# Kernel tuning notes

Measured on AMD Instinct MI355X. Metric: run time of the kernel, lower is better.

The kernel has to match this reference:

```python
import jax, jax.numpy as jnp
import numpy as np

TOK_DIM = 512
POS_DIM = 512
N_HEADS = 16
HEAD_DIM = 64
D_MODEL = 1024
INNER = N_HEADS * HEAD_DIM
B, T = 4, 2048


def setup_inputs() -> dict:
    key = jax.random.key(0)
    ks = jax.random.split(key, 5)
    s = 0.02
    return {
        "x": jax.random.normal(ks[0], (B, T, TOK_DIM + POS_DIM), dtype=jnp.float32),
        "Wq": jax.random.normal(ks[1], (POS_DIM, INNER), dtype=jnp.float32) * s,
        "Wk": jax.random.normal(ks[2], (POS_DIM, INNER), dtype=jnp.float32) * s,
        "Wv": jax.random.normal(ks[3], (TOK_DIM, INNER), dtype=jnp.float32) * s,
        "Wo": jax.random.normal(ks[4], (INNER, D_MODEL), dtype=jnp.float32) * s,
    }


def reference(x, Wq, Wk, Wv, Wo):
    b, t, _ = x.shape
    x_tok = x[:, :, :TOK_DIM]
    x_pos = x[:, :, TOK_DIM:]
    # project and split heads: [B, H, T, Dh]
    q = (x_pos @ Wq).reshape(b, t, N_HEADS, HEAD_DIM).transpose(0, 2, 1, 3)
    k = (x_pos @ Wk).reshape(b, t, N_HEADS, HEAD_DIM).transpose(0, 2, 1, 3)
    v = (x_tok @ Wv).reshape(b, t, N_HEADS, HEAD_DIM).transpose(0, 2, 1, 3)
    att = jnp.einsum("bhqd,bhkd->bhqk", q, k) / jnp.sqrt(jnp.float32(HEAD_DIM))
    causal = jnp.tril(jnp.ones((t, t), dtype=bool))
    att = jnp.where(causal, att, -jnp.inf)
    att = jax.nn.softmax(att, axis=-1)
    out = jnp.einsum("bhqk,bhkd->bhqd", att, v)
    out = out.transpose(0, 2, 1, 3).reshape(b, t, INNER)
    return out @ Wo
```

## Files before the change

### kernel.cpp

```cpp
#include <hip/hip_runtime.h>
#include <stdint.h>


typedef unsigned short u16;
typedef __bf16 bf16;
typedef bf16 bf16x8 __attribute__((ext_vector_type(8)));
typedef u16 u16x8 __attribute__((ext_vector_type(8)));
typedef u16 u16x4 __attribute__((ext_vector_type(4)));
typedef float f32x4 __attribute__((ext_vector_type(4)));
typedef uint32_t u32x4 __attribute__((ext_vector_type(4)));

__device__ __forceinline__ u16 cvt_bf16(float f) {
  uint32_t u = __builtin_bit_cast(uint32_t, f);
  u += 0x7FFFu + ((u >> 16) & 1u);
  return (u16)(u >> 16);
}

__device__ __forceinline__ uint32_t pack2_bf16(float lo, float hi) {
  uint32_t a = __builtin_bit_cast(uint32_t, lo) + 0x8000u;
  uint32_t b = __builtin_bit_cast(uint32_t, hi) + 0x8000u;
  return __builtin_amdgcn_perm(b, a, 0x07060302u);
}

__device__ __forceinline__ f32x4 mfma_bf(bf16x8 a, bf16x8 b, f32x4 c) {
  return __builtin_amdgcn_mfma_f32_16x16x32_bf16(a, b, c, 0, 0, 0);
}

typedef __attribute__((address_space(1))) const uint32_t g_u32;
typedef __attribute__((address_space(3))) uint32_t l_u32;
__device__ __forceinline__ void gload16(const u16* g, u16* l) {
  __builtin_amdgcn_global_load_lds((g_u32*)g, (l_u32*)l, 16, 0, 0);
}

__global__ __launch_bounds__(256) void prep_x(
    const float* __restrict__ x, u16* __restrict__ xtok,
    u16* __restrict__ xpos) {
  int idx = blockIdx.x * 256 + threadIdx.x;
  int row = idx >> 8;
  int c4 = (idx & 255) * 4;
  float4 v = *(const float4*)(x + (size_t)row * 1024 + c4);
  u16x4 b = {cvt_bf16(v.x), cvt_bf16(v.y), cvt_bf16(v.z), cvt_bf16(v.w)};
  u16* dst = (c4 < 512) ? (xtok + (size_t)row * 512 + c4)
                        : (xpos + (size_t)row * 512 + c4 - 512);
  *(u16x4*)dst = b;
}

__global__ __launch_bounds__(256) void prep_w(
    const float* __restrict__ Wq, const float* __restrict__ Wk,
    const float* __restrict__ Wv, const float* __restrict__ Wo,
    u16* __restrict__ Wt, u16* __restrict__ WoT) {
  const int z = blockIdx.z;
  const float* src = (z == 0) ? Wq : (z == 1) ? Wk : (z == 2) ? Wv : Wo;
  const int K = (z == 3) ? 1024 : 512;
  u16* dst = (z == 3) ? WoT : (Wt + (size_t)z * 1024 * 512);
  const int k0 = blockIdx.y * 64, n0 = blockIdx.x * 64;
  if (k0 >= K) return;
  __shared__ u16 T[64][68];
  const int tid = threadIdx.x;
  const int r = tid >> 4, c = (tid & 15) * 4;
#pragma unroll
  for (int i = 0; i < 4; i++) {
    float4 v = *(const float4*)(src + (size_t)(k0 + r + i * 16) * 1024 + n0 + c);
    u16x4 b = {cvt_bf16(v.x), cvt_bf16(v.y), cvt_bf16(v.z), cvt_bf16(v.w)};
    *(u16x4*)&T[r + i * 16][c] = b;
  }
  __syncthreads();
#pragma unroll
  for (int i = 0; i < 4; i++) {
    int n = r + i * 16;
    u16x4 v;
#pragma unroll
    for (int j = 0; j < 4; j++) v[j] = T[c + j][n];
    *(u16x4*)(dst + (size_t)(n0 + n) * K + k0 + c) = v;
  }
}

__global__ __launch_bounds__(256) void gemm_qkv(
    const u16* __restrict__ xtok, const u16* __restrict__ xpos,
    const u16* __restrict__ Wt, u16* __restrict__ qkv,
    u16* __restrict__ vperm) {
  const int z = blockIdx.z;
  const u16* A = (z == 2) ? xtok : xpos;
  const u16* Bt = Wt + (size_t)z * 1024 * 512;
  u16* outp = qkv + (size_t)z * (64u * 2048u * 64u);
  const float osc = (z == 0) ? 0.18033688011112042f : 1.0f;

  const int m0 = blockIdx.y * 128;
  const int n0 = blockIdx.x * 128;
  const int tid = threadIdx.x;
  const int lane = tid & 63;
  const int w = tid >> 6;
  const int wm = (w & 1) * 64;
  const int wn = (w >> 1) * 64;
  const int mrow = lane & 15;
  const int quad = lane >> 4;

  __shared__ __align__(16) u16 Ash[128 * 32];
  __shared__ __align__(16) u16 Bsh[128 * 32];

  f32x4 acc[4][4];
#pragma unroll
  for (int i = 0; i < 4; i++)
#pragma unroll
    for (int j = 0; j < 4; j++) acc[i][j] = (f32x4){0.f, 0.f, 0.f, 0.f};

  const int sr = w * 16 + (lane >> 2);
  const int sc = (lane & 3) * 8;
  const u16* gA = A + (size_t)(m0 + sr) * 512 + sc;
  const u16* gB = Bt + (size_t)(n0 + sr) * 512 + sc;
  u16* lA = Ash + sr * 32 + sc;
  u16* lB = Bsh + sr * 32 + sc;

  for (int kb = 0; kb < 512; kb += 32) {
    __syncthreads();
    gload16(gA + kb, lA);
    gload16(gA + 64 * 512 + kb, lA + 64 * 32);
    gload16(gB + kb, lB);
    gload16(gB + 64 * 512 + kb, lB + 64 * 32);
    __syncthreads();

    bf16x8 af[4], bfr[4];
#pragma unroll
    for (int mi = 0; mi < 4; mi++)
      af[mi] = *(const bf16x8*)(Ash + (wm + mi * 16 + mrow) * 32 + quad * 8);
#pragma unroll
    for (int ni = 0; ni < 4; ni++)
      bfr[ni] = *(const bf16x8*)(Bsh + (wn + ni * 16 + mrow) * 32 + quad * 8);
#pragma unroll
    for (int mi = 0; mi < 4; mi++)
#pragma unroll
      for (int ni = 0; ni < 4; ni++)
        acc[mi][ni] = mfma_bf(af[mi], bfr[ni], acc[mi][ni]);
  }

  if (z != 2) {
#pragma unroll
    for (int mi = 0; mi < 4; mi++)
#pragma unroll
      for (int ni = 0; ni < 4; ni++)
#pragma unroll
        for (int r = 0; r < 4; r++) {
          int m = m0 + wm + mi * 16 + quad * 4 + r;
          int n = n0 + wn + ni * 16 + mrow;
          int bb = m >> 11, t = m & 2047;
          int h = n >> 6, d = n & 63;
          outp[(((size_t)(bb * 16 + h)) * 2048 + t) * 64 + d] =
              cvt_bf16(acc[mi][ni][r] * osc);
        }
  } else {
#pragma unroll
    for (int mi = 0; mi < 4; mi++)
#pragma unroll
      for (int ni = 0; ni < 4; ni++)
#pragma unroll
        for (int r = 0; r < 4; r++) {
          int m = m0 + wm + mi * 16 + quad * 4 + r;
          int n = n0 + wn + ni * 16 + mrow;
          int bb = m >> 11, t = m & 2047;
          int h = n >> 6, d = n & 63;
          int k6 = t & 63;
          int pos = (k6 & 32) + ((k6 >> 4) & 1) * 4 + ((k6 >> 2) & 3) * 8 +
                    (k6 & 3);
          vperm[(((size_t)(bb * 16 + h)) * 64 + d) * 2048 + (t & ~63) + pos] =
              cvt_bf16(acc[mi][ni][r]);
        }
  }
}

__global__ __launch_bounds__(256, 4) void attn(
    const u16* __restrict__ qkv, const u16* __restrict__ vperm,
    u16* __restrict__ aout) {
  const int bh = blockIdx.x;
  const int sp = blockIdx.y;
  const int bb = bh >> 4, h = bh & 15;
  const u16* Qp = qkv + (size_t)bh * (2048 * 64);
  const u16* Kp = qkv + (size_t)(64 + bh) * (2048 * 64);
  const u16* Vp = vperm + (size_t)bh * (64 * 2048);

  __shared__ __align__(16) u16 Ksh0[64 * 32], Ksh1[64 * 32];
  __shared__ __align__(16) u16 Vsh0[64 * 32], Vsh1[64 * 32];
  __shared__ __align__(16) u16 Osh[4][16][72];

  const int tid = threadIdx.x;
  const int lane = tid & 63;
  const int w = tid >> 6;
  const int mrow = lane & 15;
  const int quad = lane >> 4;
  const int srow = w * 16 + (lane >> 2);
  const int sc = (lane & 3) * 8;

  const u16x8 onesu = {0x3F80, 0x3F80, 0x3F80, 0x3F80,
                       0x3F80, 0x3F80, 0x3F80, 0x3F80};
  const bf16x8 ones = __builtin_bit_cast(bf16x8, onesu);

  const u16* kgb = Kp + (size_t)srow * 64 + sc;
  const u16* vgb = Vp + (size_t)srow * 2048 + sc;

  for (int half = 0; half < 2; ++half) {
    const int qt = (half == 0) ? sp : 31 - sp;
    const int q0 = qt * 64;
    const int nk = qt + 1;

    const u16* qrow = Qp + (size_t)(q0 + w * 16 + mrow) * 64 + quad * 8;
    const bf16x8 qf0 = *(const bf16x8*)qrow;
    const bf16x8 qf1 = *(const bf16x8*)(qrow + 32);
    f32x4 o[4], ol;
#pragma unroll
    for (int dt = 0; dt < 4; ++dt) o[dt] = (f32x4){0.f, 0.f, 0.f, 0.f};
    ol = (f32x4){0.f, 0.f, 0.f, 0.f};

    u16x8 ka0 = *(const u16x8*)kgb;
    u16x8 ka1 = *(const u16x8*)(kgb + 32);
    u16x8 va0 = *(const u16x8*)vgb;
    u16x8 va1 = *(const u16x8*)(vgb + 32);

    for (int it = 0; it < nk; ++it) {
      __syncthreads();
      *(u16x8*)(Ksh0 + srow * 32 + sc) = ka0;
      *(u16x8*)(Ksh1 + srow * 32 + sc) = ka1;
      *(u16x8*)(Vsh0 + srow * 32 + sc) = va0;
      *(u16x8*)(Vsh1 + srow * 32 + sc) = va1;
      __syncthreads();

      if (it + 1 < nk) {
        const int kn = (it + 1) * 64;
        ka0 = *(const u16x8*)(kgb + (size_t)kn * 64);
        ka1 = *(const u16x8*)(kgb + (size_t)kn * 64 + 32);
        va0 = *(const u16x8*)(vgb + kn);
        va1 = *(const u16x8*)(vgb + kn + 32);
      }

      const int k0 = it * 64;
      f32x4 s[4];
#pragma unroll
      for (int nt = 0; nt < 4; ++nt) {
        bf16x8 kf0 = *(const bf16x8*)(Ksh0 + (nt * 16 + mrow) * 32 + quad * 8);
        bf16x8 kf1 = *(const bf16x8*)(Ksh1 + (nt * 16 + mrow) * 32 + quad * 8);
        f32x4 zz = (f32x4){0.f, 0.f, 0.f, 0.f};
        zz = mfma_bf(kf0, qf0, zz);
        zz = mfma_bf(kf1, qf1, zz);
        s[nt] = zz;
      }

      if (it == nk - 1) {
        const int q = q0 + w * 16 + mrow;
#pragma unroll
        for (int nt = 0; nt < 4; ++nt)
#pragma unroll
          for (int r = 0; r < 4; ++r)
            if (k0 + nt * 16 + quad * 4 + r > q) s[nt][r] = -1e30f;
      }
#pragma unroll
      for (int nt = 0; nt < 4; ++nt)
#pragma unroll
        for (int r = 0; r < 4; ++r)
          s[nt][r] = __builtin_amdgcn_exp2f(s[nt][r]);

      u32x4 w0 = {pack2_bf16(s[0][0], s[0][1]), pack2_bf16(s[0][2], s[0][3]),
                  pack2_bf16(s[1][0], s[1][1]), pack2_bf16(s[1][2], s[1][3])};
      u32x4 w1 = {pack2_bf16(s[2][0], s[2][1]), pack2_bf16(s[2][2], s[2][3]),
                  pack2_bf16(s[3][0], s[3][1]), pack2_bf16(s[3][2], s[3][3])};
      bf16x8 pf0 = __builtin_bit_cast(bf16x8, w0);
      bf16x8 pf1 = __builtin_bit_cast(bf16x8, w1);

      ol = mfma_bf(ones, pf0, ol);
      ol = mfma_bf(ones, pf1, ol);
#pragma unroll
      for (int dt = 0; dt < 4; ++dt) {
        bf16x8 vf0 = *(const bf16x8*)(Vsh0 + (dt * 16 + mrow) * 32 + quad * 8);
        bf16x8 vf1 = *(const bf16x8*)(Vsh1 + (dt * 16 + mrow) * 32 + quad * 8);
        o[dt] = mfma_bf(vf0, pf0, o[dt]);
        o[dt] = mfma_bf(vf1, pf1, o[dt]);
      }
    }

    const float inv = 1.f / ol[0];
#pragma unroll
    for (int dt = 0; dt < 4; ++dt)
#pragma unroll
      for (int r = 0; r < 4; ++r)
        Osh[w][mrow][dt * 16 + quad * 4 + r] = cvt_bf16(o[dt][r] * inv);
#pragma unroll
    for (int p = 0; p < 2; ++p) {
      int ql = (lane >> 3) + 8 * p;
      int ch = lane & 7;
      u16x8 v = *(const u16x8*)&Osh[w][ql][ch * 8];
      int t = q0 + w * 16 + ql;
      *(u16x8*)(aout + ((size_t)(bb * 2048 + t)) * 1024 + h * 64 + ch * 8) = v;
    }
  }
}

__global__ __launch_bounds__(256) void gemm_out(
    const u16* __restrict__ Am, const u16* __restrict__ WoT,
    float* __restrict__ out) {
  const int m0 = blockIdx.y * 128;
  const int n0 = blockIdx.x * 128;
  const int tid = threadIdx.x;
  const int lane = tid & 63;
  const int w = tid >> 6;
  const int wm = (w & 1) * 64;
  const int wn = (w >> 1) * 64;
  const int mrow = lane & 15;
  const int quad = lane >> 4;

  __shared__ __align__(16) u16 Ash[128 * 32];
  __shared__ __align__(16) u16 Bsh[128 * 32];

  f32x4 acc[4][4];
#pragma unroll
  for (int i = 0; i < 4; i++)
#pragma unroll
    for (int j = 0; j < 4; j++) acc[i][j] = (f32x4){0.f, 0.f, 0.f, 0.f};

  const int sr = w * 16 + (lane >> 2);
  const int sc = (lane & 3) * 8;
  const u16* gA = Am + (size_t)(m0 + sr) * 1024 + sc;
  const u16* gB = WoT + (size_t)(n0 + sr) * 1024 + sc;
  u16* lA = Ash + sr * 32 + sc;
  u16* lB = Bsh + sr * 32 + sc;

  for (int kb = 0; kb < 1024; kb += 32) {
    __syncthreads();
    gload16(gA + kb, lA);
    gload16(gA + 64 * 1024 + kb, lA + 64 * 32);
    gload16(gB + kb, lB);
    gload16(gB + 64 * 1024 + kb, lB + 64 * 32);
    __syncthreads();

    bf16x8 af[4], bfr[4];
#pragma unroll
    for (int mi = 0; mi < 4; mi++)
      af[mi] = *(const bf16x8*)(Ash + (wm + mi * 16 + mrow) * 32 + quad * 8);
#pragma unroll
    for (int ni = 0; ni < 4; ni++)
      bfr[ni] = *(const bf16x8*)(Bsh + (wn + ni * 16 + mrow) * 32 + quad * 8);
#pragma unroll
    for (int mi = 0; mi < 4; mi++)
#pragma unroll
      for (int ni = 0; ni < 4; ni++)
        acc[mi][ni] = mfma_bf(af[mi], bfr[ni], acc[mi][ni]);
  }

#pragma unroll
  for (int mi = 0; mi < 4; mi++)
#pragma unroll
    for (int ni = 0; ni < 4; ni++)
#pragma unroll
      for (int r = 0; r < 4; r++) {
        int m = m0 + wm + mi * 16 + quad * 4 + r;
        int n = n0 + wn + ni * 16 + mrow;
        out[(size_t)m * 1024 + n] = acc[mi][ni][r];
      }
}

extern "C" void kernel_launch(void* const* d_in, const int* in_sizes, int n_in,
                              void* d_out, int out_size, void* d_ws, size_t ws_size,
                              hipStream_t stream) {
  const float* x  = (const float*)d_in[0];
  const float* Wq = (const float*)d_in[1];
  const float* Wk = (const float*)d_in[2];
  const float* Wv = (const float*)d_in[3];
  const float* Wo = (const float*)d_in[4];

  u16* qkv   = (u16*)d_ws;
  u16* vperm = qkv + (size_t)3 * 64 * 2048 * 64;
  u16* aout  = vperm + (size_t)64 * 64 * 2048;
  u16* xtok  = aout + (size_t)8192 * 1024;
  u16* xpos  = xtok + (size_t)8192 * 512;
  u16* Wt    = xpos + (size_t)8192 * 512;
  u16* WoT   = Wt + (size_t)3 * 1024 * 512;
  float* out = (float*)d_out;

  prep_x<<<dim3(8192), dim3(256), 0, stream>>>(x, xtok, xpos);
  prep_w<<<dim3(16, 16, 4), dim3(256), 0, stream>>>(Wq, Wk, Wv, Wo, Wt, WoT);
  gemm_qkv<<<dim3(8, 64, 3), dim3(256), 0, stream>>>(xtok, xpos, Wt, qkv, vperm);
  attn<<<dim3(64, 16), dim3(256), 0, stream>>>(qkv, vperm, aout);
  gemm_out<<<dim3(8, 64), dim3(256), 0, stream>>>(aout, WoT, out);
}
```

Measured before the change: 223.6 us.

## Split attention into one block per query tile with padded LDS and vectorized V stores

The attention kernel drops the paired-tile scheme (sp and 31-sp in one block) and launches one block per query tile, giving 2048 blocks with launch bounds raised to 8 per SIMD and a single shared buffer reused for the output staging. The LDS rows for K and V are padded from 32 to 36 elements, and the load mapping is changed so lanes cover 16 rows by 4 chunks, to cut bank conflicts. The gemm_qkv V-permuted epilogue now writes four consecutive bf16 values as one 8-byte store instead of four scalar stores. The trade-off is worse load balance, since block work now grows from 1 to 32 KV tiles, and the launch bound of 8 may force register spills.

```diff
diff --git a/kernel.cpp b/kernel.cpp
--- a/kernel.cpp
+++ b/kernel.cpp
@@ -151,143 +151,145 @@
 #pragma unroll
     for (int mi = 0; mi < 4; mi++)
 #pragma unroll
-      for (int ni = 0; ni < 4; ni++)
-#pragma unroll
-        for (int r = 0; r < 4; r++) {
-          int m = m0 + wm + mi * 16 + quad * 4 + r;
-          int n = n0 + wn + ni * 16 + mrow;
-          int bb = m >> 11, t = m & 2047;
-          int h = n >> 6, d = n & 63;
-          int k6 = t & 63;
-          int pos = (k6 & 32) + ((k6 >> 4) & 1) * 4 + ((k6 >> 2) & 3) * 8 +
-                    (k6 & 3);
-          vperm[(((size_t)(bb * 16 + h)) * 64 + d) * 2048 + (t & ~63) + pos] =
-              cvt_bf16(acc[mi][ni][r]);
-        }
-  }
-}
-
-__global__ __launch_bounds__(256, 4) void attn(
+      for (int ni = 0; ni < 4; ni++) {
+        int m = m0 + wm + mi * 16 + quad * 4;
+        int n = n0 + wn + ni * 16 + mrow;
+        int bb = m >> 11, t = m & 2047;
+        int h = n >> 6, d = n & 63;
+        int k6 = t & 63;
+        int pos = (k6 & 32) + ((k6 >> 4) & 1) * 4 + ((k6 >> 2) & 3) * 8;
+        u16x4 v = {cvt_bf16(acc[mi][ni][0]), cvt_bf16(acc[mi][ni][1]),
+                   cvt_bf16(acc[mi][ni][2]), cvt_bf16(acc[mi][ni][3])};
+        *(u16x4*)(vperm + (((size_t)(bb * 16 + h)) * 64 + d) * 2048 +
+                  (t & ~63) + pos) = v;
+      }
+  }
+}
+
+__global__ __launch_bounds__(256, 8) void attn(
     const u16* __restrict__ qkv, const u16* __restrict__ vperm,
     u16* __restrict__ aout) {
   const int bh = blockIdx.x;
-  const int sp = blockIdx.y;
+  const int qt = blockIdx.y;
   const int bb = bh >> 4, h = bh & 15;
   const u16* Qp = qkv + (size_t)bh * (2048 * 64);
   const u16* Kp = qkv + (size_t)(64 + bh) * (2048 * 64);
   const u16* Vp = vperm + (size_t)bh * (64 * 2048);
 
-  __shared__ __align__(16) u16 Ksh0[64 * 32], Ksh1[64 * 32];
-  __shared__ __align__(16) u16 Vsh0[64 * 32], Vsh1[64 * 32];
-  __shared__ __align__(16) u16 Osh[4][16][72];
+  __shared__ __align__(16) u16 S[9216];
+  u16* Ksh0 = S;
+  u16* Ksh1 = S + 2304;
+  u16* Vsh0 = S + 4608;
+  u16* Vsh1 = S + 6912;
+  u16* Osh  = S;
 
   const int tid = threadIdx.x;
   const int lane = tid & 63;
   const int w = tid >> 6;
   const int mrow = lane & 15;
   const int quad = lane >> 4;
-  const int srow = w * 16 + (lane >> 2);
-  const int sc = (lane & 3) * 8;
+  const int srow = w * 16 + (lane & 15);
+  const int sch = (lane >> 4) * 8;
 
   const u16x8 onesu = {0x3F80, 0x3F80, 0x3F80, 0x3F80,
                        0x3F80, 0x3F80, 0x3F80, 0x3F80};
   const bf16x8 ones = __builtin_bit_cast(bf16x8, onesu);
 
-  const u16* kgb = Kp + (size_t)srow * 64 + sc;
-  const u16* vgb = Vp + (size_t)srow * 2048 + sc;
-
-  for (int half = 0; half < 2; ++half) {
-    const int qt = (half == 0) ? sp : 31 - sp;
-    const int q0 = qt * 64;
-    const int nk = qt + 1;
-
-    const u16* qrow = Qp + (size_t)(q0 + w * 16 + mrow) * 64 + quad * 8;
-    const bf16x8 qf0 = *(const bf16x8*)qrow;
-    const bf16x8 qf1 = *(const bf16x8*)(qrow + 32);
-    f32x4 o[4], ol;
-#pragma unroll
-    for (int dt = 0; dt < 4; ++dt) o[dt] = (f32x4){0.f, 0.f, 0.f, 0.f};
-    ol = (f32x4){0.f, 0.f, 0.f, 0.f};
-
-    u16x8 ka0 = *(const u16x8*)kgb;
-    u16x8 ka1 = *(const u16x8*)(kgb + 32);
-    u16x8 va0 = *(const u16x8*)vgb;
-    u16x8 va1 = *(const u16x8*)(vgb + 32);
-
-    for (int it = 0; it < nk; ++it) {
-      __syncthreads();
-      *(u16x8*)(Ksh0 + srow * 32 + sc) = ka0;
-      *(u16x8*)(Ksh1 + srow * 32 + sc) = ka1;
-      *(u16x8*)(Vsh0 + srow * 32 + sc) = va0;
-      *(u16x8*)(Vsh1 + srow * 32 + sc) = va1;
-      __syncthreads();
-
-      if (it + 1 < nk) {
-        const int kn = (it + 1) * 64;
-        ka0 = *(const u16x8*)(kgb + (size_t)kn * 64);
-        ka1 = *(const u16x8*)(kgb + (size_t)kn * 64 + 32);
-        va0 = *(const u16x8*)(vgb + kn);
-        va1 = *(const u16x8*)(vgb + kn + 32);
-      }
-
-      const int k0 = it * 64;
-      f32x4 s[4];
-#pragma unroll
-      for (int nt = 0; nt < 4; ++nt) {
-        bf16x8 kf0 = *(const bf16x8*)(Ksh0 + (nt * 16 + mrow) * 32 + quad * 8);
-        bf16x8 kf1 = *(const bf16x8*)(Ksh1 + (nt * 16 + mrow) * 32 + quad * 8);
-        f32x4 zz = (f32x4){0.f, 0.f, 0.f, 0.f};
-        zz = mfma_bf(kf0, qf0, zz);
-        zz = mfma_bf(kf1, qf1, zz);
-        s[nt] = zz;
-      }
-
-      if (it == nk - 1) {
-        const int q = q0 + w * 16 + mrow;
-#pragma unroll
-        for (int nt = 0; nt < 4; ++nt)
-#pragma unroll
-          for (int r = 0; r < 4; ++r)
-            if (k0 + nt * 16 + quad * 4 + r > q) s[nt][r] = -1e30f;
-      }
+  const u16* kgb = Kp + (size_t)srow * 64 + sch;
+  const u16* vgb = Vp + (size_t)srow * 2048 + sch;
+  const int lidx = srow * 36 + sch;
+
+  const int q0 = qt * 64;
+  const int nk = qt + 1;
+
+  const u16* qrow = Qp + (size_t)(q0 + w * 16 + mrow) * 64 + quad * 8;
+  const bf16x8 qf0 = *(const bf16x8*)qrow;
+  const bf16x8 qf1 = *(const bf16x8*)(qrow + 32);
+  f32x4 o[4], ol;
+#pragma unroll
+  for (int dt = 0; dt < 4; ++dt) o[dt] = (f32x4){0.f, 0.f, 0.f, 0.f};
+  ol = (f32x4){0.f, 0.f, 0.f, 0.f};
+
+  u16x8 ka0 = *(const u16x8*)kgb;
+  u16x8 ka1 = *(const u16x8*)(kgb + 32);
+  u16x8 va0 = *(const u16x8*)vgb;
+  u16x8 va1 = *(const u16x8*)(vgb + 32);
+
+  for (int it = 0; it < nk; ++it) {
+    __syncthreads();
+    *(u16x8*)(Ksh0 + lidx) = ka0;
+    *(u16x8*)(Ksh1 + lidx) = ka1;
+    *(u16x8*)(Vsh0 + lidx) = va0;
+    *(u16x8*)(Vsh1 + lidx) = va1;
+    __syncthreads();
+
+    if (it + 1 < nk) {
+      const int kn = (it + 1) * 64;
+      ka0 = *(const u16x8*)(kgb + (size_t)kn * 64);
+      ka1 = *(const u16x8*)(kgb + (size_t)kn * 64 + 32);
+      va0 = *(const u16x8*)(vgb + kn);
+      va1 = *(const u16x8*)(vgb + kn + 32);
+    }
+
+    const int k0 = it * 64;
+    f32x4 s[4];
+#pragma unroll
+    for (int nt = 0; nt < 4; ++nt) {
+      bf16x8 kf0 = *(const bf16x8*)(Ksh0 + (nt * 16 + mrow) * 36 + quad * 8);
+      bf16x8 kf1 = *(const bf16x8*)(Ksh1 + (nt * 16 + mrow) * 36 + quad * 8);
+      f32x4 zz = (f32x4){0.f, 0.f, 0.f, 0.f};
+      zz = mfma_bf(kf0, qf0, zz);
+      zz = mfma_bf(kf1, qf1, zz);
+      s[nt] = zz;
+    }
+
+    if (it == nk - 1) {
+      const int q = q0 + w * 16 + mrow;
 #pragma unroll
       for (int nt = 0; nt < 4; ++nt)
 #pragma unroll
         for (int r = 0; r < 4; ++r)
-          s[nt][r] = __builtin_amdgcn_exp2f(s[nt][r]);
-
-      u32x4 w0 = {pack2_bf16(s[0][0], s[0][1]), pack2_bf16(s[0][2], s[0][3]),
-                  pack2_bf16(s[1][0], s[1][1]), pack2_bf16(s[1][2], s[1][3])};
-      u32x4 w1 = {pack2_bf16(s[2][0], s[2][1]), pack2_bf16(s[2][2], s[2][3]),
-                  pack2_bf16(s[3][0], s[3][1]), pack2_bf16(s[3][2], s[3][3])};
-      bf16x8 pf0 = __builtin_bit_cast(bf16x8, w0);
-      bf16x8 pf1 = __builtin_bit_cast(bf16x8, w1);
-
-      ol = mfma_bf(ones, pf0, ol);
-      ol = mfma_bf(ones, pf1, ol);
-#pragma unroll
-      for (int dt = 0; dt < 4; ++dt) {
-        bf16x8 vf0 = *(const bf16x8*)(Vsh0 + (dt * 16 + mrow) * 32 + quad * 8);
-        bf16x8 vf1 = *(const bf16x8*)(Vsh1 + (dt * 16 + mrow) * 32 + quad * 8);
-        o[dt] = mfma_bf(vf0, pf0, o[dt]);
-        o[dt] = mfma_bf(vf1, pf1, o[dt]);
-      }
+          if (k0 + nt * 16 + quad * 4 + r > q) s[nt][r] = -1e30f;
     }
-
-    const float inv = 1.f / ol[0];
-#pragma unroll
-    for (int dt = 0; dt < 4; ++dt)
+#pragma unroll
+    for (int nt = 0; nt < 4; ++nt)
 #pragma unroll
       for (int r = 0; r < 4; ++r)
-        Osh[w][mrow][dt * 16 + quad * 4 + r] = cvt_bf16(o[dt][r] * inv);
-#pragma unroll
-    for (int p = 0; p < 2; ++p) {
-      int ql = (lane >> 3) + 8 * p;
-      int ch = lane & 7;
-      u16x8 v = *(const u16x8*)&Osh[w][ql][ch * 8];
-      int t = q0 + w * 16 + ql;
-      *(u16x8*)(aout + ((size_t)(bb * 2048 + t)) * 1024 + h * 64 + ch * 8) = v;
+        s[nt][r] = __builtin_amdgcn_exp2f(s[nt][r]);
+
+    u32x4 w0 = {pack2_bf16(s[0][0], s[0][1]), pack2_bf16(s[0][2], s[0][3]),
+                pack2_bf16(s[1][0], s[1][1]), pack2_bf16(s[1][2], s[1][3])};
+    u32x4 w1 = {pack2_bf16(s[2][0], s[2][1]), pack2_bf16(s[2][2], s[2][3]),
+                pack2_bf16(s[3][0], s[3][1]), pack2_bf16(s[3][2], s[3][3])};
+    bf16x8 pf0 = __builtin_bit_cast(bf16x8, w0);
+    bf16x8 pf1 = __builtin_bit_cast(bf16x8, w1);
+
+    ol = mfma_bf(ones, pf0, ol);
+    ol = mfma_bf(ones, pf1, ol);
+#pragma unroll
+    for (int dt = 0; dt < 4; ++dt) {
+      bf16x8 vf0 = *(const bf16x8*)(Vsh0 + (dt * 16 + mrow) * 36 + quad * 8);
+      bf16x8 vf1 = *(const bf16x8*)(Vsh1 + (dt * 16 + mrow) * 36 + quad * 8);
+      o[dt] = mfma_bf(vf0, pf0, o[dt]);
+      o[dt] = mfma_bf(vf1, pf1, o[dt]);
     }
+  }
+
+  __syncthreads();
+  const float inv = 1.f / ol[0];
+#pragma unroll
+  for (int dt = 0; dt < 4; ++dt)
+#pragma unroll
+    for (int r = 0; r < 4; ++r)
+      Osh[(w * 16 + mrow) * 72 + dt * 16 + quad * 4 + r] =
+          cvt_bf16(o[dt][r] * inv);
+#pragma unroll
+  for (int p = 0; p < 2; ++p) {
+    int ql = (lane >> 3) + 8 * p;
+    int ch = lane & 7;
+    u16x8 v = *(const u16x8*)(Osh + (w * 16 + ql) * 72 + ch * 8);
+    int t = q0 + w * 16 + ql;
+    *(u16x8*)(aout + ((size_t)(bb * 2048 + t)) * 1024 + h * 64 + ch * 8) = v;
   }
 }
 
@@ -375,6 +377,6 @@
   prep_x<<<dim3(8192), dim3(256), 0, stream>>>(x, xtok, xpos);
   prep_w<<<dim3(16, 16, 4), dim3(256), 0, stream>>>(Wq, Wk, Wv, Wo, Wt, WoT);
   gemm_qkv<<<dim3(8, 64, 3), dim3(256), 0, stream>>>(xtok, xpos, Wt, qkv, vperm);
-  attn<<<dim3(64, 16), dim3(256), 0, stream>>>(qkv, vperm, aout);
+  attn<<<dim3(64, 32), dim3(256), 0, stream>>>(qkv, vperm, aout);
   gemm_out<<<dim3(8, 64), dim3(256), 0, stream>>>(aout, WoT, out);
 }
```

Result: slower. 497.0 us (+122.3%).
